# Performance work log

Hardware: AMD Instinct MI355X
Metric: run time of the kernel (lower is better)

Reference implementation:

```python
import jax, jax.numpy as jnp
import numpy as np

MARKER = 50251
BETA_FLOOR = 0.1
LOCAL_SCALE = 0.3
EPS = 1e-6
WINDOW = 256

B, T, D, H, K, V = 4, 1024, 1024, 16, 64, 64
HD = D // H  # SWA head dim


def setup_inputs() -> dict:
    key = jax.random.key(0)
    ks = jax.random.split(key, 16)
    p = lambda i, shape: jax.random.normal(ks[i], shape, jnp.float32) * 0.02
    return dict(
        x=jax.random.normal(ks[0], (B, T, D), jnp.float32),
        initial_state=jnp.zeros((B, H, K, V), jnp.float32),
        W_k=p(1, (D, H * K)),
        W_v=p(2, (D, H * V)),
        W_gdn_o=p(3, (H * V, D)),
        W_beta=p(4, (D, H)), b_beta=jnp.full((H,), -2.0, jnp.float32),
        W_g=p(5, (D, H)), b_g=jnp.full((H,), 2.0, jnp.float32),
        W_lq=p(6, (D, D)), W_lk=p(7, (D, D)), W_lv=p(8, (D, D)),
        W_swa_o=p(9, (D, D)),
        W_ret_o=p(10, (H * V, D)),
        W_gate=p(11, (D, H)), b_gate=jnp.ones((H,), jnp.float32),
        norm_w=jnp.ones((D,), jnp.float32),
        input_ids=jax.random.randint(ks[12], (B, T), 0, 50257, jnp.int32),
    )


def _delta_scan(k, v, beta, g, S0):
    # gated delta rule:  Sd = g_t * S_{t-1};  S_t = Sd + beta_t * k_t (v_t - k_t Sd);  o_t = k_t S_t
    # k:[B,Tm,H,K]  v:[B,Tm,H,V]  beta,g:[B,Tm,H]  S0:[B,H,K,V]
    def step(S, inp):
        kt, vt, bt, gt = inp  # [B,H,K],[B,H,V],[B,H],[B,H]
        Sd = gt[..., None, None] * S
        err = vt - jnp.einsum('bhk,bhkv->bhv', kt, Sd)
        Sn = Sd + bt[..., None, None] * (kt[..., None] * err[:, :, None, :])
        ot = jnp.einsum('bhk,bhkv->bhv', kt, Sn)
        return Sn, ot
    Sf, o = jax.lax.scan(step, S0, (k.transpose(1, 0, 2, 3), v.transpose(1, 0, 2, 3),
                                    beta.transpose(1, 0, 2), g.transpose(1, 0, 2)))
    return o.transpose(1, 0, 2, 3), Sf  # [B,Tm,H,V], [B,H,K,V]


def _forward(x, initial_state, W_k, W_v, W_gdn_o, W_beta, b_beta, W_g, b_g,
             W_lq, W_lk, W_lv, W_swa_o, W_ret_o, W_gate, b_gate, norm_w, input_ids):
    # RMSNorm
    rms = jnp.sqrt(jnp.mean(x * x, axis=-1, keepdims=True) + EPS)
    xn = x / rms * norm_w

    # shared L2-normalized keys and values
    k_shared = (xn @ W_k).reshape(B, T, H, K)
    k_shared = k_shared / jnp.maximum(jnp.linalg.norm(k_shared, axis=-1, keepdims=True), 1e-12)
    v_full = (xn @ W_v).reshape(B, T, H, V)

    # shifted-value GDN inputs (predict next token's value)
    k = k_shared[:, :-1]
    v = v_full[:, 1:]
    beta = jax.nn.sigmoid(xn[:, :-1] @ W_beta + b_beta)  # [B,T-1,H]
    g = jax.nn.sigmoid(xn[:, :-1] @ W_g + b_g)
    marker = (input_ids[:, :-1] == MARKER)[..., None]
    beta = beta * (BETA_FLOOR + (1.0 - BETA_FLOOR) * marker.astype(beta.dtype))

    o, Sf = _delta_scan(k, v, beta, g, initial_state)
    gdn_out = jnp.concatenate([jnp.zeros((B, 1, H, V), o.dtype), o], axis=1)
    gdn_out = gdn_out.reshape(B, T, H * V) @ W_gdn_o  # [B,T,D]

    # sliding-window attention (fallback masked-softmax path)
    q = (xn @ W_lq).reshape(B, T, H, HD).transpose(0, 2, 1, 3)
    kl = (xn @ W_lk).reshape(B, T, H, HD).transpose(0, 2, 1, 3)
    vl = (xn @ W_lv).reshape(B, T, H, HD).transpose(0, 2, 1, 3)
    scale = K ** (-0.5)
    i = jnp.arange(T)[:, None]
    j = jnp.arange(T)[None, :]
    allowed = (j <= i) & (j >= i - WINDOW)  # causal within window
    attn = jnp.einsum('bhqd,bhkd->bhqk', q, kl) * scale
    attn = jnp.where(allowed, attn, -jnp.inf)
    probs = jax.nn.softmax(attn, axis=-1)
    local = jnp.einsum('bhqk,bhkd->bhqd', probs, vl).transpose(0, 2, 1, 3).reshape(B, T, D)
    local_out = LOCAL_SCALE * (local @ W_swa_o)  # eval mode

    # retrieval from final state with shared keys as queries
    retrieved = jnp.einsum('bhkv,bthk->bthv', Sf, k_shared).reshape(B, T, H * V)
    retrieval_out = retrieved @ W_ret_o
    gate = jax.nn.sigmoid(xn @ W_gate + b_gate)  # [B,T,H]
    retrieval_out = jnp.mean(gate, axis=-1, keepdims=True) * retrieval_out

    return x + gdn_out + local_out + retrieval_out


def reference(x, initial_state, W_k, W_v, W_gdn_o, W_beta, b_beta, W_g, b_g,
              W_lq, W_lk, W_lv, W_swa_o, W_ret_o, W_gate, b_gate, norm_w, input_ids):
    return _forward(x, initial_state, W_k, W_v, W_gdn_o, W_beta, b_beta, W_g, b_g,
                    W_lq, W_lk, W_lv, W_swa_o, W_ret_o, W_gate, b_gate, norm_w, input_ids)
```

## Files before the change

### kernel.cpp

```cpp
#include <hip/hip_runtime.h>
#include <hip/hip_bf16.h>

#define BB 4
#define TT 1024
#define DD 1024
#define HH 16
#define KK 64
#define VV 64
#define WIN 256
#define MARKER_ID 50251
#define PSA 5120
#define PSB 3072
#define NPROJ 5248

typedef short bfrag8 __attribute__((ext_vector_type(8)));
typedef float f32x4 __attribute__((ext_vector_type(4)));

static __device__ __forceinline__ unsigned short f2bf(float f) {
  __hip_bfloat16 h = __float2bfloat16(f);
  union { __hip_bfloat16 h; unsigned short u; } cv;
  cv.h = h;
  return cv.u;
}
static __device__ __forceinline__ float bf2f(unsigned short u) {
  union { unsigned int i; float f; } c;
  c.i = ((unsigned int)u) << 16;
  return c.f;
}
static __device__ __forceinline__ void gld_lds16(const unsigned short* g,
                                                 unsigned short* l) {
  __builtin_amdgcn_global_load_lds(
      (const __attribute__((address_space(1))) void*)g,
      (__attribute__((address_space(3))) void*)l, 16, 0, 0);
}

__global__ __launch_bounds__(256) void rmsnorm_kernel(
    const float* __restrict__ x, const float* __restrict__ nw,
    unsigned short* __restrict__ xnb) {
  int row = blockIdx.x;
  int tid = threadIdx.x;
  const float4* xr = (const float4*)(x + (size_t)row * DD);
  float4 v = xr[tid];
  float ss = v.x * v.x + v.y * v.y + v.z * v.z + v.w * v.w;
#pragma unroll
  for (int off = 32; off; off >>= 1) ss += __shfl_xor(ss, off);
  __shared__ float red[4];
  int wid = tid >> 6;
  if ((tid & 63) == 0) red[wid] = ss;
  __syncthreads();
  float tot = red[0] + red[1] + red[2] + red[3];
  float inv = 1.0f / sqrtf(tot * (1.0f / DD) + 1e-6f);
  const float4* wr = (const float4*)nw;
  float4 wv = wr[tid];
  ushort4 o;
  o.x = f2bf(v.x * inv * wv.x);
  o.y = f2bf(v.y * inv * wv.y);
  o.z = f2bf(v.z * inv * wv.z);
  o.w = f2bf(v.w * inv * wv.w);
  *(ushort4*)&xnb[(size_t)row * DD + tid * 4] = o;
}

__global__ __launch_bounds__(256) void convert_wt_kernel(
    const float* W0, const float* W1, const float* W2, const float* W3,
    const float* W4, const float* W5, const float* W6, const float* W7,
    const float* Wb, const float* Wg, const float* Wgt,
    unsigned short* C5, unsigned short* C3) {
  int tid = threadIdx.x;
  if (blockIdx.z == 8) {
    if (blockIdx.x != 0) return;
    int k0 = blockIdx.y * 64;
    for (int e = tid; e < 3 * 16 * 64; e += 256) {
      int w = e >> 10;
      int h = (e >> 6) & 15;
      int kk = e & 63;
      const float* Ws = (w == 0) ? Wb : (w == 1) ? Wg : Wgt;
      C5[(size_t)(5120 + w * 16 + h) * 1024 + k0 + kk] =
          f2bf(Ws[(size_t)(k0 + kk) * 16 + h]);
    }
    for (int e = tid; e < 80 * 64; e += 256) {
      int r = e >> 6, kk = e & 63;
      C5[(size_t)(5168 + r) * 1024 + k0 + kk] = 0;
    }
    return;
  }
  const float* W;
  unsigned short* T;
  int stride;
  float scale = 1.f;
  switch (blockIdx.z) {
    case 0: W = W0; T = C5 + 0 * 1024 * 1024; stride = 1024; break;
    case 1: W = W1; T = C5 + 1 * 1024 * 1024; stride = 1024; break;
    case 2: W = W2; T = C5 + 2 * 1024 * 1024; stride = 1024; break;
    case 3: W = W3; T = C5 + 3 * 1024 * 1024; stride = 1024; break;
    case 4: W = W4; T = C5 + 4 * 1024 * 1024; stride = 1024; break;
    case 5: W = W5; T = C3 + 0; stride = PSB; break;
    case 6: W = W6; T = C3 + 1024; stride = PSB; scale = 0.3f; break;
    default: W = W7; T = C3 + 2048; stride = PSB; break;
  }
  __shared__ float Ts[64][68];
  int n0 = blockIdx.x * 64, k0 = blockIdx.y * 64;
#pragma unroll
  for (int p = 0; p < 4; ++p) {
    int e = p * 256 + tid;
    int k = e >> 4, nq = e & 15;
    float4 w = *(const float4*)&W[(size_t)(k0 + k) * 1024 + n0 + nq * 4];
    Ts[nq * 4 + 0][k] = w.x;
    Ts[nq * 4 + 1][k] = w.y;
    Ts[nq * 4 + 2][k] = w.z;
    Ts[nq * 4 + 3][k] = w.w;
  }
  __syncthreads();
#pragma unroll
  for (int p = 0; p < 4; ++p) {
    int e = p * 256 + tid;
    int n = e >> 4, kq = e & 15;
    float4 v = *(const float4*)&Ts[n][kq * 4];
    ushort4 u;
    u.x = f2bf(v.x * scale);
    u.y = f2bf(v.y * scale);
    u.z = f2bf(v.z * scale);
    u.w = f2bf(v.w * scale);
    *(ushort4*)&T[(size_t)(n0 + n) * stride + k0 + kq * 4] = u;
  }
}

__global__ __launch_bounds__(256) void gemm_out_kernel(
    const unsigned short* __restrict__ A, const unsigned short* __restrict__ BT,
    float* __restrict__ C, const float* __restrict__ addp, int M, int N,
    int K) {
  __shared__ unsigned short As[128][32];
  __shared__ unsigned short Bs[64][32];
  int flat = blockIdx.y * gridDim.x + blockIdx.x;
  int xcd = flat & 7, local = flat >> 3;
  int m0 = (xcd * 4 + (local & 3)) * 128;
  int n0 = (local >> 2) * 64;
  int tid = threadIdx.x;
  int wave = tid >> 6, lane = tid & 63;
  int wm = wave * 32;
  int r16 = lane & 15, quad = lane >> 4;
  int lrow = lane >> 2, lcol = (lane & 3) * 8;

  f32x4 acc[2][4];
#pragma unroll
  for (int i = 0; i < 2; ++i)
#pragma unroll
    for (int j = 0; j < 4; ++j) acc[i][j] = {0.f, 0.f, 0.f, 0.f};

  for (int kt = 0; kt < K; kt += 32) {
    __syncthreads();
#pragma unroll
    for (int q = 0; q < 2; ++q) {
      int rb = (wave * 2 + q) * 16;
      gld_lds16(&A[(size_t)(m0 + rb + lrow) * K + kt + lcol], &As[rb][0]);
    }
    {
      int rb = wave * 16;
      gld_lds16(&BT[(size_t)(n0 + rb + lrow) * K + kt + lcol], &Bs[rb][0]);
    }
    __syncthreads();
    bfrag8 af[2], bq[4];
#pragma unroll
    for (int i = 0; i < 2; ++i)
      af[i] = *(const bfrag8*)&As[wm + i * 16 + r16][quad * 8];
#pragma unroll
    for (int j = 0; j < 4; ++j)
      bq[j] = *(const bfrag8*)&Bs[j * 16 + r16][quad * 8];
#pragma unroll
    for (int i = 0; i < 2; ++i)
#pragma unroll
      for (int j = 0; j < 4; ++j)
        acc[i][j] = __builtin_amdgcn_mfma_f32_16x16x32_bf16(af[i], bq[j],
                                                            acc[i][j], 0, 0, 0);
  }
#pragma unroll
  for (int i = 0; i < 2; ++i) {
#pragma unroll
    for (int r = 0; r < 4; ++r) {
      int row = m0 + wm + i * 16 + quad * 4 + r;
#pragma unroll
      for (int j = 0; j < 4; ++j) {
        int col = n0 + j * 16 + r16;
        size_t idx = (size_t)row * N + col;
        C[idx] = addp[idx] + acc[i][j][r];
      }
    }
  }
}

__global__ __launch_bounds__(256) void gemm_proj_kernel(
    const unsigned short* __restrict__ A, const unsigned short* __restrict__ BT,
    unsigned short* __restrict__ PALL, float* __restrict__ SPRJ) {
  const int K = 1024;
  __shared__ unsigned short As[128][32];
  __shared__ unsigned short Bs[128][32];
  int flat = blockIdx.y * gridDim.x + blockIdx.x;
  int xcd = flat & 7, local = flat >> 3;
  int mi = local / 41, ni = local % 41;
  int m0 = (xcd * 4 + mi) * 128;
  int n0 = ni * 128;
  int tid = threadIdx.x;
  int wave = tid >> 6, lane = tid & 63;
  int wm = (wave & 1) * 64, wn = (wave >> 1) * 64;
  int r16 = lane & 15, quad = lane >> 4;
  int lrow = lane >> 2, lcol = (lane & 3) * 8;

  f32x4 acc[4][4];
#pragma unroll
  for (int i = 0; i < 4; ++i)
#pragma unroll
    for (int j = 0; j < 4; ++j) acc[i][j] = {0.f, 0.f, 0.f, 0.f};

  for (int kt = 0; kt < K; kt += 32) {
    __syncthreads();
#pragma unroll
    for (int q = 0; q < 2; ++q) {
      int rb = (wave * 2 + q) * 16;
      gld_lds16(&A[(size_t)(m0 + rb + lrow) * K + kt + lcol], &As[rb][0]);
      gld_lds16(&BT[(size_t)(n0 + rb + lrow) * K + kt + lcol], &Bs[rb][0]);
    }
    __syncthreads();
    bfrag8 af[4], bq[4];
#pragma unroll
    for (int i = 0; i < 4; ++i) {
      af[i] = *(const bfrag8*)&As[wm + i * 16 + r16][quad * 8];
      bq[i] = *(const bfrag8*)&Bs[wn + i * 16 + r16][quad * 8];
    }
#pragma unroll
    for (int i = 0; i < 4; ++i)
#pragma unroll
      for (int j = 0; j < 4; ++j)
        acc[i][j] = __builtin_amdgcn_mfma_f32_16x16x32_bf16(af[i], bq[j],
                                                            acc[i][j], 0, 0, 0);
  }
  bool gates = (n0 >= 5120);
#pragma unroll
  for (int i = 0; i < 4; ++i) {
#pragma unroll
    for (int r = 0; r < 4; ++r) {
      int row = m0 + wm + i * 16 + quad * 4 + r;
#pragma unroll
      for (int j = 0; j < 4; ++j) {
        int col = n0 + wn + j * 16 + r16;
        if (!gates)
          PALL[(size_t)row * PSA + col] = f2bf(acc[i][j][r]);
        else
          SPRJ[(size_t)row * 128 + col - 5120] = acc[i][j][r];
      }
    }
  }
}

__global__ __launch_bounds__(256) void gates_kernel(
    const float* __restrict__ SPRJ, const float* __restrict__ bb,
    const float* __restrict__ bg, const float* __restrict__ bgt,
    const int* __restrict__ ids, float* __restrict__ beta,
    float* __restrict__ g, float* __restrict__ mg) {
  int row = blockIdx.x * 4 + (threadIdx.x >> 6);
  int lane = threadIdx.x & 63;
  if (lane < 48) {
    int h = lane & 15;
    float v = SPRJ[(size_t)row * 128 + lane];
    float bias = (lane < 16) ? bb[h] : (lane < 32) ? bg[h] : bgt[h];
    float s = 1.f / (1.f + __expf(-(v + bias)));
    if (lane < 16) {
      float mk = (ids[row] == MARKER_ID) ? 1.f : 0.1f;
      beta[(size_t)row * 16 + h] = s * mk;
    } else if (lane < 32) {
      g[(size_t)row * 16 + h] = s;
    } else {
      float sum = s;
#pragma unroll
      for (int off = 1; off < 16; off <<= 1) sum += __shfl_xor(sum, off);
      if (lane == 32) mg[row] = sum * (1.f / 16.f);
    }
  }
}

__global__ __launch_bounds__(256) void knorm_kernel(
    unsigned short* __restrict__ pall) {
  int w = blockIdx.x * 4 + (threadIdx.x >> 6);
  int lane = threadIdx.x & 63;
  size_t addr = (size_t)(w >> 4) * PSA + (w & 15) * 64 + lane;
  float v = bf2f(pall[addr]);
  float ss = v * v;
#pragma unroll
  for (int off = 32; off; off >>= 1) ss += __shfl_xor(ss, off);
  float n = sqrtf(ss);
  n = fmaxf(n, 1e-12f);
  pall[addr] = f2bf(v / n);
}

__global__ __launch_bounds__(256) void attn_mfma_kernel(
    const unsigned short* __restrict__ PALL, unsigned short* __restrict__ ACAT) {
  __shared__ unsigned short Qs[64][72];
  __shared__ unsigned short Ks[64][72];
  __shared__ unsigned short Vt[64][72];
  __shared__ unsigned short Ps[64][72];
  int qb = blockIdx.x * 64;
  int bh = blockIdx.y;
  int h = bh & 15, b = bh >> 4;
  int tid = threadIdx.x, lane = tid & 63, wave = tid >> 6;
  int r16 = lane & 15, quad = lane >> 4;
  int m0w = wave * 16;
  const unsigned short* Qg = PALL + (size_t)b * TT * PSA + 2048 + h * 64;
  const unsigned short* Kg = Qg + 1024;
  const unsigned short* Vg = Qg + 2048;
  int sr = tid >> 2, sq = tid & 3;
  {
    *(uint4*)&Qs[sr][sq * 16] =
        *(const uint4*)&Qg[(size_t)(qb + sr) * PSA + sq * 16];
    *(uint4*)&Qs[sr][sq * 16 + 8] =
        *(const uint4*)&Qg[(size_t)(qb + sr) * PSA + sq * 16 + 8];
  }
  float m[4], l[4];
  f32x4 o[4];
#pragma unroll
  for (int r = 0; r < 4; ++r) {
    m[r] = -1e30f;
    l[r] = 0.f;
    o[r] = {0.f, 0.f, 0.f, 0.f};
  }
  int kt0 = qb - (int)WIN;
  if (kt0 < 0) kt0 = 0;

  for (int kt = kt0; kt <= qb; kt += 64) {
    __syncthreads();
    {
      *(uint4*)&Ks[sr][sq * 16] =
          *(const uint4*)&Kg[(size_t)(kt + sr) * PSA + sq * 16];
      *(uint4*)&Ks[sr][sq * 16 + 8] =
          *(const uint4*)&Kg[(size_t)(kt + sr) * PSA + sq * 16 + 8];
      union { uint4 u4[2]; unsigned short s[16]; } vv;
      vv.u4[0] = *(const uint4*)&Vg[(size_t)(kt + sr) * PSA + sq * 16];
      vv.u4[1] = *(const uint4*)&Vg[(size_t)(kt + sr) * PSA + sq * 16 + 8];
#pragma unroll
      for (int i = 0; i < 16; ++i) Vt[sq * 16 + i][sr] = vv.s[i];
    }
    __syncthreads();
    bfrag8 af0 = *(const bfrag8*)&Qs[m0w + r16][quad * 8];
    bfrag8 af1 = *(const bfrag8*)&Qs[m0w + r16][quad * 8 + 32];
    f32x4 s[4];
#pragma unroll
    for (int j = 0; j < 4; ++j) s[j] = {0.f, 0.f, 0.f, 0.f};
#pragma unroll
    for (int j = 0; j < 4; ++j) {
      bfrag8 b0 = *(const bfrag8*)&Ks[j * 16 + r16][quad * 8];
      bfrag8 b1 = *(const bfrag8*)&Ks[j * 16 + r16][quad * 8 + 32];
      s[j] = __builtin_amdgcn_mfma_f32_16x16x32_bf16(af0, b0, s[j], 0, 0, 0);
      s[j] = __builtin_amdgcn_mfma_f32_16x16x32_bf16(af1, b1, s[j], 0, 0, 0);
    }
    bool oldest = (kt == qb - (int)WIN);
    bool newest = (kt == qb);
#pragma unroll
    for (int r = 0; r < 4; ++r) {
      int il = m0w + quad * 4 + r;
      float sv[4];
#pragma unroll
      for (int j = 0; j < 4; ++j) {
        int jl = j * 16 + r16;
        float v = s[j][r] * 0.125f;
        if (oldest && jl < il) v = -1e30f;
        if (newest && jl > il) v = -1e30f;
        sv[j] = v;
      }
      float mx = fmaxf(fmaxf(sv[0], sv[1]), fmaxf(sv[2], sv[3]));
#pragma unroll
      for (int off = 1; off < 16; off <<= 1) mx = fmaxf(mx, __shfl_xor(mx, off));
      float mn = fmaxf(m[r], mx);
      float al = __expf(m[r] - mn);
      m[r] = mn;
      float rs = 0.f;
#pragma unroll
      for (int j = 0; j < 4; ++j) {
        float p = __expf(sv[j] - mn);
        rs += p;
        Ps[il][j * 16 + r16] = f2bf(p);
      }
#pragma unroll
      for (int off = 1; off < 16; off <<= 1) rs += __shfl_xor(rs, off);
      l[r] = l[r] * al + rs;
#pragma unroll
      for (int j = 0; j < 4; ++j) o[j][r] *= al;
    }
    bfrag8 pa0 = *(const bfrag8*)&Ps[m0w + r16][quad * 8];
    bfrag8 pa1 = *(const bfrag8*)&Ps[m0w + r16][quad * 8 + 32];
#pragma unroll
    for (int j = 0; j < 4; ++j) {
      bfrag8 v0 = *(const bfrag8*)&Vt[j * 16 + r16][quad * 8];
      bfrag8 v1 = *(const bfrag8*)&Vt[j * 16 + r16][quad * 8 + 32];
      o[j] = __builtin_amdgcn_mfma_f32_16x16x32_bf16(pa0, v0, o[j], 0, 0, 0);
      o[j] = __builtin_amdgcn_mfma_f32_16x16x32_bf16(pa1, v1, o[j], 0, 0, 0);
    }
  }
#pragma unroll
  for (int r = 0; r < 4; ++r) {
    int row = m0w + quad * 4 + r;
    float inv = 1.f / l[r];
#pragma unroll
    for (int j = 0; j < 4; ++j) {
      ACAT[((size_t)(b * TT + qb + row)) * PSB + 1024 + h * 64 + j * 16 + r16] =
          f2bf(o[j][r] * inv);
    }
  }
}

__global__ __launch_bounds__(256) void scan_phaseA(
    const unsigned short* __restrict__ PALL, const float* __restrict__ beta,
    const float* __restrict__ g, unsigned short* __restrict__ UFg,
    unsigned short* __restrict__ Zg, unsigned short* __restrict__ Pg,
    unsigned short* __restrict__ Qg, float* __restrict__ Ag) {
  __shared__ unsigned short Kc[64][72];
  __shared__ unsigned short KTb[64][72];
  __shared__ float Vc[64][68];
  __shared__ float Msv[64][68];
  __shared__ unsigned short UFT[64][72];
  __shared__ unsigned short ZTl[64][72];
  __shared__ float aArr[64], iaArr[64], bArr[64], baArr[64], sKT[64];
  __shared__ float aCs;

  int c = blockIdx.x, bh = blockIdx.y;
  int b = bh >> 4, h = bh & 15;
  int tc = c * 64;
  int tid = threadIdx.x, lane = tid & 63, wave = tid >> 6;
  int r16 = lane & 15, quad = lane >> 4;
  int m0w = wave * 16;
  size_t bhc = (size_t)bh * 16 + c;

  const unsigned short* kbase = PALL + ((size_t)b * TT) * PSA + h * 64;
  const unsigned short* vbase = kbase + 1024;
  const float* bbase = beta + ((size_t)b * TT) * HH + h;
  const float* gbase = g + ((size_t)b * TT) * HH + h;

  if (tid < 64) {
    int ts = tc + tid;
    bool pad = (ts > 1022);
    float gv = pad ? 1.f : gbase[(size_t)ts * HH];
    float bv = pad ? 0.f : bbase[(size_t)ts * HH];
    float p = gv;
#pragma unroll
    for (int o = 1; o < 64; o <<= 1) {
      float t = __shfl_up(p, o);
      if (lane >= o) p *= t;
    }
    aArr[tid] = p;
    iaArr[tid] = 1.f / p;
    bArr[tid] = bv;
    baArr[tid] = bv * p;
    float aC = __shfl(p, 63);
    sKT[tid] = aC / p;
    if (tid == 0) aCs = aC;
    Ag[bhc * 64 + tid] = p;
  }
  __syncthreads();
  {
    int r = tid >> 2, q = tid & 3;
    int ts = tc + r;
    float skt = sKT[r];
    union { uint4 u4[2]; unsigned short s[16]; } kv;
    kv.u4[0] = *(const uint4*)&kbase[(size_t)ts * PSA + q * 16];
    kv.u4[1] = *(const uint4*)&kbase[(size_t)ts * PSA + q * 16 + 8];
    *(uint4*)&Kc[r][q * 16] = kv.u4[0];
    *(uint4*)&Kc[r][q * 16 + 8] = kv.u4[1];
#pragma unroll
    for (int i = 0; i < 16; ++i)
      KTb[q * 16 + i][r] = f2bf(bf2f(kv.s[i]) * skt);
    if (ts <= 1022) {
      union { uint4 u4[2]; unsigned short s[16]; } vv;
      vv.u4[0] = *(const uint4*)&vbase[(size_t)(ts + 1) * PSA + q * 16];
      vv.u4[1] = *(const uint4*)&vbase[(size_t)(ts + 1) * PSA + q * 16 + 8];
#pragma unroll
      for (int i = 0; i < 16; ++i) Vc[r][q * 16 + i] = bf2f(vv.s[i]);
    } else {
#pragma unroll
      for (int i = 0; i < 16; ++i) Vc[r][q * 16 + i] = 0.f;
    }
  }
  __syncthreads();
  {
    bfrag8 af0 = *(const bfrag8*)&Kc[m0w + r16][quad * 8];
    bfrag8 af1 = *(const bfrag8*)&Kc[m0w + r16][quad * 8 + 32];
    f32x4 acc1[4];
#pragma unroll
    for (int j = 0; j < 4; ++j) acc1[j] = {0.f, 0.f, 0.f, 0.f};
#pragma unroll
    for (int j = 0; j < 4; ++j) {
      bfrag8 k0 = *(const bfrag8*)&Kc[j * 16 + r16][quad * 8];
      bfrag8 k1 = *(const bfrag8*)&Kc[j * 16 + r16][quad * 8 + 32];
      acc1[j] = __builtin_amdgcn_mfma_f32_16x16x32_bf16(af0, k0, acc1[j], 0, 0, 0);
      acc1[j] = __builtin_amdgcn_mfma_f32_16x16x32_bf16(af1, k1, acc1[j], 0, 0, 0);
    }
#pragma unroll
    for (int j = 0; j < 4; ++j) {
#pragma unroll
      for (int r = 0; r < 4; ++r) {
        int row = m0w + quad * 4 + r;
        int col = j * 16 + r16;
        Msv[row][col] =
            (col < row) ? bArr[row] * aArr[row] * iaArr[col] * acc1[j][r] : 0.f;
      }
    }
  }
  __syncthreads();
  if (wave < 2) {
    float u[64];
    if (wave == 0) {
#pragma unroll
      for (int t = 0; t < 64; ++t) u[t] = bArr[t] * Vc[t][lane];
    } else {
#pragma unroll
      for (int t = 0; t < 64; ++t) u[t] = baArr[t] * bf2f(Kc[t][lane]);
    }
#pragma unroll
    for (int t = 1; t < 64; ++t) {
      float a0 = 0.f, a1 = 0.f, a2 = 0.f, a3 = 0.f;
#pragma unroll
      for (int s4 = 0; s4 * 4 < t; ++s4) {
        float4 mr = *(const float4*)&Msv[t][s4 * 4];
        a0 = fmaf(mr.x, u[s4 * 4 + 0], a0);
        a1 = fmaf(mr.y, u[s4 * 4 + 1], a1);
        a2 = fmaf(mr.z, u[s4 * 4 + 2], a2);
        a3 = fmaf(mr.w, u[s4 * 4 + 3], a3);
      }
      u[t] -= (a0 + a1) + (a2 + a3);
    }
    unsigned short* Tls = (wave == 0) ? &UFT[lane][0] : &ZTl[lane][0];
#pragma unroll
    for (int t2 = 0; t2 < 32; ++t2) {
      unsigned int pk = (unsigned int)f2bf(u[2 * t2]) |
                        ((unsigned int)f2bf(u[2 * t2 + 1]) << 16);
      *(unsigned int*)&Tls[2 * t2] = pk;
    }
    unsigned short* Gn = (wave == 0) ? UFg : Zg;
#pragma unroll
    for (int t = 0; t < 64; ++t) {
      Gn[(bhc * 64 + t) * 64 + lane] = f2bf(u[t]);
    }
  }
  __syncthreads();
  {
    bfrag8 af0 = *(const bfrag8*)&KTb[m0w + r16][quad * 8];
    bfrag8 af1 = *(const bfrag8*)&KTb[m0w + r16][quad * 8 + 32];
    f32x4 accp[4], accq[4];
#pragma unroll
    for (int j = 0; j < 4; ++j) {
      accp[j] = {0.f, 0.f, 0.f, 0.f};
      accq[j] = {0.f, 0.f, 0.f, 0.f};
    }
#pragma unroll
    for (int j = 0; j < 4; ++j) {
      bfrag8 z0 = *(const bfrag8*)&ZTl[j * 16 + r16][quad * 8];
      bfrag8 z1 = *(const bfrag8*)&ZTl[j * 16 + r16][quad * 8 + 32];
      accp[j] = __builtin_amdgcn_mfma_f32_16x16x32_bf16(af0, z0, accp[j], 0, 0, 0);
      accp[j] = __builtin_amdgcn_mfma_f32_16x16x32_bf16(af1, z1, accp[j], 0, 0, 0);
      bfrag8 u0 = *(const bfrag8*)&UFT[j * 16 + r16][quad * 8];
      bfrag8 u1 = *(const bfrag8*)&UFT[j * 16 + r16][quad * 8 + 32];
      accq[j] = __builtin_amdgcn_mfma_f32_16x16x32_bf16(af0, u0, accq[j], 0, 0, 0);
      accq[j] = __builtin_amdgcn_mfma_f32_16x16x32_bf16(af1, u1, accq[j], 0, 0, 0);
    }
    float aC = aCs;
#pragma unroll
    for (int j = 0; j < 4; ++j) {
#pragma unroll
      for (int r = 0; r < 4; ++r) {
        int row = m0w + quad * 4 + r;
        int col = j * 16 + r16;
        float pv = ((row == col) ? aC : 0.f) - accp[j][r];
        Pg[bhc * 4096 + (size_t)row * 64 + col] = f2bf(pv);
        Qg[bhc * 4096 + (size_t)row * 64 + col] = f2bf(accq[j][r]);
      }
    }
  }
}

__global__ __launch_bounds__(256) void scan_phaseB(
    const float* __restrict__ S0, const unsigned short* __restrict__ Pg,
    const unsigned short* __restrict__ Qg, unsigned short* __restrict__ SinTg,
    float* __restrict__ Sf, unsigned short* __restrict__ ACAT) {
  __shared__ unsigned short STb[64][72];
  __shared__ unsigned short Pl[64][72];
  int bh = blockIdx.x;
  int b = bh >> 4, h = bh & 15;
  int tid = threadIdx.x, lane = tid & 63, wave = tid >> 6;
  int r16 = lane & 15, quad = lane >> 4;
  int m0w = wave * 16;
  int rr = tid >> 2, qq = tid & 3;
  {
    const float* s0p = S0 + (size_t)bh * 4096;
#pragma unroll
    for (int i = 0; i < 4; ++i) {
      float4 sv = *(const float4*)&s0p[rr * 64 + qq * 16 + i * 4];
      STb[qq * 16 + i * 4 + 0][rr] = f2bf(sv.x);
      STb[qq * 16 + i * 4 + 1][rr] = f2bf(sv.y);
      STb[qq * 16 + i * 4 + 2][rr] = f2bf(sv.z);
      STb[qq * 16 + i * 4 + 3][rr] = f2bf(sv.w);
    }
    if (tid < 64) ACAT[((size_t)b * TT) * PSB + h * 64 + tid] = 0;
  }
  for (int c = 0; c < 16; ++c) {
    size_t bhc = (size_t)bh * 16 + c;
    __syncthreads();
    {
      uint4 s0v = *(const uint4*)&STb[rr][qq * 16];
      uint4 s1v = *(const uint4*)&STb[rr][qq * 16 + 8];
      *(uint4*)&SinTg[bhc * 4096 + (size_t)rr * 64 + qq * 16] = s0v;
      *(uint4*)&SinTg[bhc * 4096 + (size_t)rr * 64 + qq * 16 + 8] = s1v;
      uint4 p0 = *(const uint4*)&Pg[bhc * 4096 + (size_t)rr * 64 + qq * 16];
      uint4 p1 = *(const uint4*)&Pg[bhc * 4096 + (size_t)rr * 64 + qq * 16 + 8];
      *(uint4*)&Pl[rr][qq * 16] = p0;
      *(uint4*)&Pl[rr][qq * 16 + 8] = p1;
    }
    __syncthreads();
    f32x4 acc[4];
#pragma unroll
    for (int j = 0; j < 4; ++j) acc[j] = {0.f, 0.f, 0.f, 0.f};
    {
      bfrag8 af0 = *(const bfrag8*)&Pl[m0w + r16][quad * 8];
      bfrag8 af1 = *(const bfrag8*)&Pl[m0w + r16][quad * 8 + 32];
#pragma unroll
      for (int j = 0; j < 4; ++j) {
        bfrag8 s0v = *(const bfrag8*)&STb[j * 16 + r16][quad * 8];
        bfrag8 s1v = *(const bfrag8*)&STb[j * 16 + r16][quad * 8 + 32];
        acc[j] = __builtin_amdgcn_mfma_f32_16x16x32_bf16(af0, s0v, acc[j], 0, 0, 0);
        acc[j] = __builtin_amdgcn_mfma_f32_16x16x32_bf16(af1, s1v, acc[j], 0, 0, 0);
      }
    }
    float snew[4][4];
#pragma unroll
    for (int j = 0; j < 4; ++j) {
#pragma unroll
      for (int r = 0; r < 4; ++r) {
        int row = m0w + quad * 4 + r;
        int col = j * 16 + r16;
        snew[j][r] = acc[j][r] + bf2f(Qg[bhc * 4096 + (size_t)row * 64 + col]);
      }
    }
    __syncthreads();
#pragma unroll
    for (int j = 0; j < 4; ++j) {
#pragma unroll
      for (int r = 0; r < 4; ++r) {
        int row = m0w + quad * 4 + r;
        int col = j * 16 + r16;
        STb[col][row] = f2bf(snew[j][r]);
        if (c == 15) Sf[(size_t)bh * 4096 + (size_t)row * 64 + col] = snew[j][r];
      }
    }
  }
}

__global__ __launch_bounds__(256) void scan_phaseC(
    const unsigned short* __restrict__ PALL,
    const unsigned short* __restrict__ UFg,
    const unsigned short* __restrict__ Zg,
    const unsigned short* __restrict__ SinTg, const float* __restrict__ Ag,
    unsigned short* __restrict__ ACAT) {
  __shared__ unsigned short Kc[64][72];
  __shared__ unsigned short SvT[64][72];
  __shared__ unsigned short Zl[64][72];
  __shared__ unsigned short Ufl[64][72];
  __shared__ unsigned short Wl[64][72];
  __shared__ unsigned short UTl[64][72];
  __shared__ float aA[64], iaA[64];

  int c = blockIdx.x, bh = blockIdx.y;
  int b = bh >> 4, h = bh & 15;
  int tc = c * 64;
  int tid = threadIdx.x, lane = tid & 63, wave = tid >> 6;
  int r16 = lane & 15, quad = lane >> 4;
  int m0w = wave * 16;
  size_t bhc = (size_t)bh * 16 + c;
  const unsigned short* kbase = PALL + ((size_t)b * TT) * PSA + h * 64;

  if (tid < 64) {
    float av = Ag[bhc * 64 + tid];
    aA[tid] = av;
    iaA[tid] = 1.f / av;
  }
  {
    int r = tid >> 2, q = tid & 3;
    int ts = tc + r;
    *(uint4*)&Kc[r][q * 16] = *(const uint4*)&kbase[(size_t)ts * PSA + q * 16];
    *(uint4*)&Kc[r][q * 16 + 8] =
        *(const uint4*)&kbase[(size_t)ts * PSA + q * 16 + 8];
    uint4 sv0 = *(const uint4*)&SinTg[bhc * 4096 + (size_t)r * 64 + q * 16];
    uint4 sv1 = *(const uint4*)&SinTg[bhc * 4096 + (size_t)r * 64 + q * 16 + 8];
    *(uint4*)&SvT[r][q * 16] = sv0;
    *(uint4*)&SvT[r][q * 16 + 8] = sv1;
    uint4 zv0 = *(const uint4*)&Zg[(bhc * 64 + r) * 64 + q * 16];
    uint4 zv1 = *(const uint4*)&Zg[(bhc * 64 + r) * 64 + q * 16 + 8];
    *(uint4*)&Zl[r][q * 16] = zv0;
    *(uint4*)&Zl[r][q * 16 + 8] = zv1;
    uint4 uv0 = *(const uint4*)&UFg[(bhc * 64 + r) * 64 + q * 16];
    uint4 uv1 = *(const uint4*)&UFg[(bhc * 64 + r) * 64 + q * 16 + 8];
    *(uint4*)&Ufl[r][q * 16] = uv0;
    *(uint4*)&Ufl[r][q * 16 + 8] = uv1;
  }
  __syncthreads();
  float op[4][4];
  {
    bfrag8 af0 = *(const bfrag8*)&Kc[m0w + r16][quad * 8];
    bfrag8 af1 = *(const bfrag8*)&Kc[m0w + r16][quad * 8 + 32];
    bfrag8 zf0 = *(const bfrag8*)&Zl[m0w + r16][quad * 8];
    bfrag8 zf1 = *(const bfrag8*)&Zl[m0w + r16][quad * 8 + 32];
    f32x4 acc1[4], acc2[4], acc3[4];
#pragma unroll
    for (int j = 0; j < 4; ++j) {
      acc1[j] = {0.f, 0.f, 0.f, 0.f};
      acc2[j] = {0.f, 0.f, 0.f, 0.f};
      acc3[j] = {0.f, 0.f, 0.f, 0.f};
    }
#pragma unroll
    for (int j = 0; j < 4; ++j) {
      bfrag8 k0 = *(const bfrag8*)&Kc[j * 16 + r16][quad * 8];
      bfrag8 k1 = *(const bfrag8*)&Kc[j * 16 + r16][quad * 8 + 32];
      acc1[j] = __builtin_amdgcn_mfma_f32_16x16x32_bf16(af0, k0, acc1[j], 0, 0, 0);
      acc1[j] = __builtin_amdgcn_mfma_f32_16x16x32_bf16(af1, k1, acc1[j], 0, 0, 0);
      bfrag8 s0 = *(const bfrag8*)&SvT[j * 16 + r16][quad * 8];
      bfrag8 s1 = *(const bfrag8*)&SvT[j * 16 + r16][quad * 8 + 32];
      acc3[j] = __builtin_amdgcn_mfma_f32_16x16x32_bf16(af0, s0, acc3[j], 0, 0, 0);
      acc3[j] = __builtin_amdgcn_mfma_f32_16x16x32_bf16(af1, s1, acc3[j], 0, 0, 0);
      acc2[j] = __builtin_amdgcn_mfma_f32_16x16x32_bf16(zf0, s0, acc2[j], 0, 0, 0);
      acc2[j] = __builtin_amdgcn_mfma_f32_16x16x32_bf16(zf1, s1, acc2[j], 0, 0, 0);
    }
#pragma unroll
    for (int j = 0; j < 4; ++j) {
#pragma unroll
      for (int r = 0; r < 4; ++r) {
        int row = m0w + quad * 4 + r;
        int col = j * 16 + r16;
        Wl[row][col] = (col <= row) ? f2bf(aA[row] * iaA[col] * acc1[j][r])
                                    : (unsigned short)0;
        float uval = bf2f(Ufl[row][col]) - acc2[j][r];
        UTl[col][row] = f2bf(uval);
        op[j][r] = aA[row] * acc3[j][r];
      }
    }
  }
  __syncthreads();
  {
    bfrag8 wf0 = *(const bfrag8*)&Wl[m0w + r16][quad * 8];
    bfrag8 wf1 = *(const bfrag8*)&Wl[m0w + r16][quad * 8 + 32];
    f32x4 acc4[4];
#pragma unroll
    for (int j = 0; j < 4; ++j) acc4[j] = {0.f, 0.f, 0.f, 0.f};
#pragma unroll
    for (int j = 0; j < 4; ++j) {
      bfrag8 u0 = *(const bfrag8*)&UTl[j * 16 + r16][quad * 8];
      bfrag8 u1 = *(const bfrag8*)&UTl[j * 16 + r16][quad * 8 + 32];
      acc4[j] = __builtin_amdgcn_mfma_f32_16x16x32_bf16(wf0, u0, acc4[j], 0, 0, 0);
      acc4[j] = __builtin_amdgcn_mfma_f32_16x16x32_bf16(wf1, u1, acc4[j], 0, 0, 0);
    }
#pragma unroll
    for (int j = 0; j < 4; ++j) {
#pragma unroll
      for (int r = 0; r < 4; ++r) {
        int row = m0w + quad * 4 + r;
        int col = j * 16 + r16;
        int ts = tc + row;
        if (ts < 1023) {
          ACAT[((size_t)b * TT + ts + 1) * PSB + h * 64 + col] =
              f2bf(op[j][r] + acc4[j][r]);
        }
      }
    }
  }
}

__global__ __launch_bounds__(256) void retrieve_kernel(
    const unsigned short* __restrict__ PALL, const float* __restrict__ Sf,
    const float* __restrict__ mg, unsigned short* __restrict__ ACAT) {
  int w = blockIdx.x * 4 + (threadIdx.x >> 6);
  int lane = threadIdx.x & 63;
  int bt = w >> 4;
  float kl = bf2f(PALL[(size_t)bt * PSA + (w & 15) * 64 + lane]);
  int b = bt >> 10;
  int bh = b * 16 + (w & 15);
  const float* sfp = Sf + (size_t)bh * 4096;
  float acc = 0.f;
#pragma unroll
  for (int k = 0; k < 64; ++k) {
    float kk = __shfl(kl, k);
    acc = fmaf(kk, sfp[k * 64 + lane], acc);
  }
  ACAT[(size_t)bt * PSB + 2048 + (w & 15) * 64 + lane] = f2bf(acc * mg[bt]);
}

extern "C" void kernel_launch(void* const* d_in, const int* in_sizes, int n_in,
                              void* d_out, int out_size, void* d_ws,
                              size_t ws_size, hipStream_t stream) {
  (void)in_sizes; (void)n_in; (void)out_size; (void)ws_size;
  const float* x       = (const float*)d_in[0];
  const float* S0      = (const float*)d_in[1];
  const float* W_k     = (const float*)d_in[2];
  const float* W_v     = (const float*)d_in[3];
  const float* W_gdn_o = (const float*)d_in[4];
  const float* W_beta  = (const float*)d_in[5];
  const float* b_beta  = (const float*)d_in[6];
  const float* W_g     = (const float*)d_in[7];
  const float* b_g     = (const float*)d_in[8];
  const float* W_lq    = (const float*)d_in[9];
  const float* W_lk    = (const float*)d_in[10];
  const float* W_lv    = (const float*)d_in[11];
  const float* W_swa_o = (const float*)d_in[12];
  const float* W_ret_o = (const float*)d_in[13];
  const float* W_gate  = (const float*)d_in[14];
  const float* b_gate  = (const float*)d_in[15];
  const float* norm_w  = (const float*)d_in[16];
  const int*   ids     = (const int*)d_in[17];
  float* out = (float*)d_out;

  char* ws = (char*)d_ws;
  size_t off = 0;
  auto allocf = [&](size_t n) {
    float* p = (float*)(ws + off);
    off += n * sizeof(float);
    return p;
  };
  auto allocu = [&](size_t n) {
    unsigned short* p = (unsigned short*)(ws + off);
    off += n * sizeof(unsigned short);
    return p;
  };
  const int M = BB * TT;
  unsigned short* XNb    = allocu((size_t)M * DD);
  unsigned short* PALL   = allocu((size_t)M * PSA);
  unsigned short* ACAT   = allocu((size_t)M * PSB);
  float*          SPRJ   = allocf((size_t)M * 128);
  unsigned short* WTcat5 = allocu((size_t)NPROJ * 1024);
  unsigned short* WTcat3 = allocu((size_t)1024 * PSB);
  float* BETA = allocf((size_t)M * HH);
  float* Gg   = allocf((size_t)M * HH);
  float* MG   = allocf((size_t)M);
  float* SF   = allocf((size_t)BB * HH * KK * VV);
  const size_t CH = (size_t)BB * HH * 16 * 64 * 64;
  unsigned short* UFg   = allocu(CH);
  unsigned short* Zg    = allocu(CH);
  unsigned short* Pg    = allocu(CH);
  unsigned short* Qg    = allocu(CH);
  unsigned short* SinTg = allocu(CH);
  float* Ag = allocf((size_t)BB * HH * 16 * 64);

  rmsnorm_kernel<<<M, 256, 0, stream>>>(x, norm_w, XNb);

  convert_wt_kernel<<<dim3(16, 16, 9), 256, 0, stream>>>(
      W_k, W_v, W_lq, W_lk, W_lv, W_gdn_o, W_swa_o, W_ret_o, W_beta, W_g,
      W_gate, WTcat5, WTcat3);

  gemm_proj_kernel<<<dim3(41, 32), 256, 0, stream>>>(XNb, WTcat5, PALL, SPRJ);

  knorm_kernel<<<(M * HH) / 4, 256, 0, stream>>>(PALL);
  gates_kernel<<<M / 4, 256, 0, stream>>>(SPRJ, b_beta, b_g, b_gate, ids, BETA,
                                          Gg, MG);

  scan_phaseA<<<dim3(16, BB * HH), 256, 0, stream>>>(PALL, BETA, Gg, UFg, Zg,
                                                     Pg, Qg, Ag);
  scan_phaseB<<<BB * HH, 256, 0, stream>>>(S0, Pg, Qg, SinTg, SF, ACAT);
  scan_phaseC<<<dim3(16, BB * HH), 256, 0, stream>>>(PALL, UFg, Zg, SinTg, Ag,
                                                     ACAT);

  attn_mfma_kernel<<<dim3(TT / 64, BB * HH), 256, 0, stream>>>(PALL, ACAT);

  retrieve_kernel<<<(M * HH) / 4, 256, 0, stream>>>(PALL, SF, MG, ACAT);

  gemm_out_kernel<<<dim3(16, 32), 256, 0, stream>>>(ACAT, WTcat3, out, x, M, DD,
                                                    3072);
}
```

Before: 425.8 us.

## Double-buffer LDS tiles in projection and output GEMMs

Both bf16 MFMA GEMM kernels now use two LDS buffers per operand. The next k-tile is issued into the spare buffer while the current tile is consumed, which removes one barrier per iteration and overlaps global-to-LDS loads with MFMA work. The projection GEMM's block-to-tile mapping also changes from div/mod by 41 to interleaving the M index in the low bits, which may improve cache reuse of B tiles. LDS use per block doubles, which could lower occupancy.

New measurement: 403.7 us. -5.2%, faster.

```diff
diff --git a/kernel.cpp b/kernel.cpp
--- a/kernel.cpp
+++ b/kernel.cpp
@@ -128,8 +128,8 @@
     const unsigned short* __restrict__ A, const unsigned short* __restrict__ BT,
     float* __restrict__ C, const float* __restrict__ addp, int M, int N,
     int K) {
-  __shared__ unsigned short As[128][32];
-  __shared__ unsigned short Bs[64][32];
+  __shared__ unsigned short As[2][128][32];
+  __shared__ unsigned short Bs[2][64][32];
   int flat = blockIdx.y * gridDim.x + blockIdx.x;
   int xcd = flat & 7, local = flat >> 3;
   int m0 = (xcd * 4 + (local & 3)) * 128;
@@ -146,25 +146,54 @@
 #pragma unroll
     for (int j = 0; j < 4; ++j) acc[i][j] = {0.f, 0.f, 0.f, 0.f};
 
-  for (int kt = 0; kt < K; kt += 32) {
-    __syncthreads();
+#pragma unroll
+  for (int q = 0; q < 2; ++q) {
+    int rb = (wave * 2 + q) * 16;
+    gld_lds16(&A[(size_t)(m0 + rb + lrow) * K + lcol], &As[0][rb][0]);
+  }
+  {
+    int rb = wave * 16;
+    gld_lds16(&BT[(size_t)(n0 + rb + lrow) * K + lcol], &Bs[0][rb][0]);
+  }
+  __syncthreads();
+
+  int cur = 0;
+  for (int kt = 32; kt < K; kt += 32) {
 #pragma unroll
     for (int q = 0; q < 2; ++q) {
       int rb = (wave * 2 + q) * 16;
-      gld_lds16(&A[(size_t)(m0 + rb + lrow) * K + kt + lcol], &As[rb][0]);
+      gld_lds16(&A[(size_t)(m0 + rb + lrow) * K + kt + lcol],
+                &As[cur ^ 1][rb][0]);
     }
     {
       int rb = wave * 16;
-      gld_lds16(&BT[(size_t)(n0 + rb + lrow) * K + kt + lcol], &Bs[rb][0]);
-    }
+      gld_lds16(&BT[(size_t)(n0 + rb + lrow) * K + kt + lcol],
+                &Bs[cur ^ 1][rb][0]);
+    }
+    bfrag8 af[2], bq[4];
+#pragma unroll
+    for (int i = 0; i < 2; ++i)
+      af[i] = *(const bfrag8*)&As[cur][wm + i * 16 + r16][quad * 8];
+#pragma unroll
+    for (int j = 0; j < 4; ++j)
+      bq[j] = *(const bfrag8*)&Bs[cur][j * 16 + r16][quad * 8];
+#pragma unroll
+    for (int i = 0; i < 2; ++i)
+#pragma unroll
+      for (int j = 0; j < 4; ++j)
+        acc[i][j] = __builtin_amdgcn_mfma_f32_16x16x32_bf16(af[i], bq[j],
+                                                            acc[i][j], 0, 0, 0);
     __syncthreads();
+    cur ^= 1;
+  }
+  {
     bfrag8 af[2], bq[4];
 #pragma unroll
     for (int i = 0; i < 2; ++i)
-      af[i] = *(const bfrag8*)&As[wm + i * 16 + r16][quad * 8];
+      af[i] = *(const bfrag8*)&As[cur][wm + i * 16 + r16][quad * 8];
 #pragma unroll
     for (int j = 0; j < 4; ++j)
-      bq[j] = *(const bfrag8*)&Bs[j * 16 + r16][quad * 8];
+      bq[j] = *(const bfrag8*)&Bs[cur][j * 16 + r16][quad * 8];
 #pragma unroll
     for (int i = 0; i < 2; ++i)
 #pragma unroll
@@ -191,11 +220,11 @@
     const unsigned short* __restrict__ A, const unsigned short* __restrict__ BT,
     unsigned short* __restrict__ PALL, float* __restrict__ SPRJ) {
   const int K = 1024;
-  __shared__ unsigned short As[128][32];
-  __shared__ unsigned short Bs[128][32];
+  __shared__ unsigned short As[2][128][32];
+  __shared__ unsigned short Bs[2][128][32];
   int flat = blockIdx.y * gridDim.x + blockIdx.x;
   int xcd = flat & 7, local = flat >> 3;
-  int mi = local / 41, ni = local % 41;
+  int mi = local & 3, ni = local >> 2;
   int m0 = (xcd * 4 + mi) * 128;
   int n0 = ni * 128;
   int tid = threadIdx.x;
@@ -210,20 +239,45 @@
 #pragma unroll
     for (int j = 0; j < 4; ++j) acc[i][j] = {0.f, 0.f, 0.f, 0.f};
 
-  for (int kt = 0; kt < K; kt += 32) {
-    __syncthreads();
+#pragma unroll
+  for (int q = 0; q < 2; ++q) {
+    int rb = (wave * 2 + q) * 16;
+    gld_lds16(&A[(size_t)(m0 + rb + lrow) * K + lcol], &As[0][rb][0]);
+    gld_lds16(&BT[(size_t)(n0 + rb + lrow) * K + lcol], &Bs[0][rb][0]);
+  }
+  __syncthreads();
+
+  int cur = 0;
+  for (int kt = 32; kt < K; kt += 32) {
 #pragma unroll
     for (int q = 0; q < 2; ++q) {
       int rb = (wave * 2 + q) * 16;
-      gld_lds16(&A[(size_t)(m0 + rb + lrow) * K + kt + lcol], &As[rb][0]);
-      gld_lds16(&BT[(size_t)(n0 + rb + lrow) * K + kt + lcol], &Bs[rb][0]);
-    }
+      gld_lds16(&A[(size_t)(m0 + rb + lrow) * K + kt + lcol],
+                &As[cur ^ 1][rb][0]);
+      gld_lds16(&BT[(size_t)(n0 + rb + lrow) * K + kt + lcol],
+                &Bs[cur ^ 1][rb][0]);
+    }
+    bfrag8 af[4], bq[4];
+#pragma unroll
+    for (int i = 0; i < 4; ++i) {
+      af[i] = *(const bfrag8*)&As[cur][wm + i * 16 + r16][quad * 8];
+      bq[i] = *(const bfrag8*)&Bs[cur][wn + i * 16 + r16][quad * 8];
+    }
+#pragma unroll
+    for (int i = 0; i < 4; ++i)
+#pragma unroll
+      for (int j = 0; j < 4; ++j)
+        acc[i][j] = __builtin_amdgcn_mfma_f32_16x16x32_bf16(af[i], bq[j],
+                                                            acc[i][j], 0, 0, 0);
     __syncthreads();
+    cur ^= 1;
+  }
+  {
     bfrag8 af[4], bq[4];
 #pragma unroll
     for (int i = 0; i < 4; ++i) {
-      af[i] = *(const bfrag8*)&As[wm + i * 16 + r16][quad * 8];
-      bq[i] = *(const bfrag8*)&Bs[wn + i * 16 + r16][quad * 8];
+      af[i] = *(const bfrag8*)&As[cur][wm + i * 16 + r16][quad * 8];
+      bq[i] = *(const bfrag8*)&Bs[cur][wn + i * 16 + r16][quad * 8];
     }
 #pragma unroll
     for (int i = 0; i < 4; ++i)
```

## Double-buffer LDS tiles in projection and output GEMMs with async prefetch

Applied to the files above, without the earlier changes.

Both bf16 MFMA GEMM kernels now keep two LDS buffers and prefetch the next k-tile with direct global-to-LDS loads while computing the current one. Partial vmcnt waits and raw s_barrier replace the two __syncthreads per iteration, so load latency overlaps the MFMA work. The projection kernel also changes its block-to-tile mapping from div/mod by 41 to bit ops. The cost is twice the LDS per block, which may reduce occupancy, and the hand-tuned waitcnt counts must match the number of outstanding loads.

Measured after the change: 386.8 us. -9.2%, faster.

```diff
diff --git a/kernel.cpp b/kernel.cpp
--- a/kernel.cpp
+++ b/kernel.cpp
@@ -128,8 +128,8 @@
     const unsigned short* __restrict__ A, const unsigned short* __restrict__ BT,
     float* __restrict__ C, const float* __restrict__ addp, int M, int N,
     int K) {
-  __shared__ unsigned short As[128][32];
-  __shared__ unsigned short Bs[64][32];
+  __shared__ unsigned short As[2][128][32];
+  __shared__ unsigned short Bs[2][64][32];
   int flat = blockIdx.y * gridDim.x + blockIdx.x;
   int xcd = flat & 7, local = flat >> 3;
   int m0 = (xcd * 4 + (local & 3)) * 128;
@@ -146,32 +146,55 @@
 #pragma unroll
     for (int j = 0; j < 4; ++j) acc[i][j] = {0.f, 0.f, 0.f, 0.f};
 
-  for (int kt = 0; kt < K; kt += 32) {
-    __syncthreads();
+  auto STAGE = [&](int buf, int kt) {
 #pragma unroll
     for (int q = 0; q < 2; ++q) {
       int rb = (wave * 2 + q) * 16;
-      gld_lds16(&A[(size_t)(m0 + rb + lrow) * K + kt + lcol], &As[rb][0]);
+      gld_lds16(&A[(size_t)(m0 + rb + lrow) * K + kt + lcol], &As[buf][rb][0]);
     }
     {
       int rb = wave * 16;
-      gld_lds16(&BT[(size_t)(n0 + rb + lrow) * K + kt + lcol], &Bs[rb][0]);
-    }
-    __syncthreads();
+      gld_lds16(&BT[(size_t)(n0 + rb + lrow) * K + kt + lcol], &Bs[buf][rb][0]);
+    }
+  };
+  auto COMPUTE = [&](int buf) {
     bfrag8 af[2], bq[4];
 #pragma unroll
     for (int i = 0; i < 2; ++i)
-      af[i] = *(const bfrag8*)&As[wm + i * 16 + r16][quad * 8];
+      af[i] = *(const bfrag8*)&As[buf][wm + i * 16 + r16][quad * 8];
 #pragma unroll
     for (int j = 0; j < 4; ++j)
-      bq[j] = *(const bfrag8*)&Bs[j * 16 + r16][quad * 8];
+      bq[j] = *(const bfrag8*)&Bs[buf][j * 16 + r16][quad * 8];
 #pragma unroll
     for (int i = 0; i < 2; ++i)
 #pragma unroll
       for (int j = 0; j < 4; ++j)
         acc[i][j] = __builtin_amdgcn_mfma_f32_16x16x32_bf16(af[i], bq[j],
                                                             acc[i][j], 0, 0, 0);
-  }
+  };
+
+  STAGE(0, 0);
+  STAGE(1, 32);
+  asm volatile("s_waitcnt vmcnt(3)" ::: "memory");
+  __builtin_amdgcn_s_barrier();
+  __builtin_amdgcn_sched_barrier(0);
+
+  int cur = 0;
+  for (int kt = 64; kt < K; kt += 32) {
+    COMPUTE(cur);
+    __builtin_amdgcn_s_barrier();
+    STAGE(cur, kt);
+    asm volatile("s_waitcnt vmcnt(3)" ::: "memory");
+    __builtin_amdgcn_s_barrier();
+    __builtin_amdgcn_sched_barrier(0);
+    cur ^= 1;
+  }
+  COMPUTE(cur);
+  asm volatile("s_waitcnt vmcnt(0)" ::: "memory");
+  __builtin_amdgcn_s_barrier();
+  __builtin_amdgcn_sched_barrier(0);
+  COMPUTE(cur ^ 1);
+
 #pragma unroll
   for (int i = 0; i < 2; ++i) {
 #pragma unroll
@@ -191,11 +214,11 @@
     const unsigned short* __restrict__ A, const unsigned short* __restrict__ BT,
     unsigned short* __restrict__ PALL, float* __restrict__ SPRJ) {
   const int K = 1024;
-  __shared__ unsigned short As[128][32];
-  __shared__ unsigned short Bs[128][32];
+  __shared__ unsigned short As[2][128][32];
+  __shared__ unsigned short Bs[2][128][32];
   int flat = blockIdx.y * gridDim.x + blockIdx.x;
   int xcd = flat & 7, local = flat >> 3;
-  int mi = local / 41, ni = local % 41;
+  int mi = local & 3, ni = local >> 2;
   int m0 = (xcd * 4 + mi) * 128;
   int n0 = ni * 128;
   int tid = threadIdx.x;
@@ -210,20 +233,20 @@
 #pragma unroll
     for (int j = 0; j < 4; ++j) acc[i][j] = {0.f, 0.f, 0.f, 0.f};
 
-  for (int kt = 0; kt < K; kt += 32) {
-    __syncthreads();
+  auto STAGE = [&](int buf, int kt) {
 #pragma unroll
     for (int q = 0; q < 2; ++q) {
       int rb = (wave * 2 + q) * 16;
-      gld_lds16(&A[(size_t)(m0 + rb + lrow) * K + kt + lcol], &As[rb][0]);
-      gld_lds16(&BT[(size_t)(n0 + rb + lrow) * K + kt + lcol], &Bs[rb][0]);
-    }
-    __syncthreads();
+      gld_lds16(&A[(size_t)(m0 + rb + lrow) * K + kt + lcol], &As[buf][rb][0]);
+      gld_lds16(&BT[(size_t)(n0 + rb + lrow) * K + kt + lcol], &Bs[buf][rb][0]);
+    }
+  };
+  auto COMPUTE = [&](int buf) {
     bfrag8 af[4], bq[4];
 #pragma unroll
     for (int i = 0; i < 4; ++i) {
-      af[i] = *(const bfrag8*)&As[wm + i * 16 + r16][quad * 8];
-      bq[i] = *(const bfrag8*)&Bs[wn + i * 16 + r16][quad * 8];
+      af[i] = *(const bfrag8*)&As[buf][wm + i * 16 + r16][quad * 8];
+      bq[i] = *(const bfrag8*)&Bs[buf][wn + i * 16 + r16][quad * 8];
     }
 #pragma unroll
     for (int i = 0; i < 4; ++i)
@@ -231,7 +254,30 @@
       for (int j = 0; j < 4; ++j)
         acc[i][j] = __builtin_amdgcn_mfma_f32_16x16x32_bf16(af[i], bq[j],
                                                             acc[i][j], 0, 0, 0);
-  }
+  };
+
+  STAGE(0, 0);
+  STAGE(1, 32);
+  asm volatile("s_waitcnt vmcnt(4)" ::: "memory");
+  __builtin_amdgcn_s_barrier();
+  __builtin_amdgcn_sched_barrier(0);
+
+  int cur = 0;
+  for (int kt = 64; kt < K; kt += 32) {
+    COMPUTE(cur);
+    __builtin_amdgcn_s_barrier();
+    STAGE(cur, kt);
+    asm volatile("s_waitcnt vmcnt(4)" ::: "memory");
+    __builtin_amdgcn_s_barrier();
+    __builtin_amdgcn_sched_barrier(0);
+    cur ^= 1;
+  }
+  COMPUTE(cur);
+  asm volatile("s_waitcnt vmcnt(0)" ::: "memory");
+  __builtin_amdgcn_s_barrier();
+  __builtin_amdgcn_sched_barrier(0);
+  COMPUTE(cur ^ 1);
+
   bool gates = (n0 >= 5120);
 #pragma unroll
   for (int i = 0; i < 4; ++i) {
```
